# Optimization experiments

Hardware: AMD Instinct MI355X
Metric: run time of the kernel (lower is better)

## Reference

```python
import jax, jax.numpy as jnp
import numpy as np

EMB = 512
HEADS = 8


def setup_inputs() -> dict:
    key = jax.random.key(0)
    ks = jax.random.split(key, 9)
    b, t, k, h = 4, 2048, EMB, HEADS
    s = 1.0 / np.sqrt(k)
    x = jax.random.normal(ks[0], (b, t, k), dtype=jnp.float32)
    Wq = jax.random.normal(ks[1], (k, h * k), dtype=jnp.float32) * s
    bq = jnp.zeros((h * k,), dtype=jnp.float32)
    Wk = jax.random.normal(ks[2], (k, h * k), dtype=jnp.float32) * s
    bk = jnp.zeros((h * k,), dtype=jnp.float32)
    Wv = jax.random.normal(ks[3], (k, h * k), dtype=jnp.float32) * s
    bv = jnp.zeros((h * k,), dtype=jnp.float32)
    Wo = jax.random.normal(ks[4], (h * k, k), dtype=jnp.float32) * (1.0 / np.sqrt(h * k))
    bo = jnp.zeros((k,), dtype=jnp.float32)
    return {"x": x, "Wq": Wq, "bq": bq, "Wk": Wk, "bk": bk,
            "Wv": Wv, "bv": bv, "Wo": Wo, "bo": bo}


def reference(x, Wq, bq, Wk, bk, Wv, bv, Wo, bo):
    b, t, k = x.shape
    h = Wq.shape[1] // k
    scale = k ** (-0.25)  # applied to both q and k, matching /= k**(1/4)
    # projections: [b,t,k] -> [b,t,h,k] -> [b,h,t,k]
    q = (x @ Wq + bq).reshape(b, t, h, k).transpose(0, 2, 1, 3) * scale
    kk = (x @ Wk + bk).reshape(b, t, h, k).transpose(0, 2, 1, 3) * scale
    v = (x @ Wv + bv).reshape(b, t, h, k).transpose(0, 2, 1, 3)
    # attention scores [b,h,t,t]
    scores = jnp.einsum('bhqk,bhsk->bhqs', q, kk)
    w = jax.nn.softmax(scores, axis=-1)
    out = jnp.einsum('bhqs,bhsk->bhqk', w, v)  # [b,h,t,k]
    out = out.transpose(0, 2, 1, 3).reshape(b, t, h * k)
    return out @ Wo + bo
```

## Files before the change

### kernel.cpp

```cpp
#include <hip/hip_runtime.h>
#include <hip/hip_bf16.h>
#include <stdint.h>

typedef __hip_bfloat16 bf16;
typedef __bf16 bf16x8 __attribute__((ext_vector_type(8)));
typedef float floatx4 __attribute__((ext_vector_type(4)));

#define AS_LDS __attribute__((address_space(3)))
#define AS_GLB __attribute__((address_space(1)))

__device__ __forceinline__ void gload_lds16(const bf16* g, bf16* l) {
    __builtin_amdgcn_global_load_lds((const AS_GLB void*)g, (AS_LDS void*)l, 16, 0, 0);
}

__global__ void probe_dtype(const float* __restrict__ x, int* __restrict__ flag) {
    __shared__ int cnt;
    if (threadIdx.x == 0) cnt = 0;
    __syncthreads();
    int ok = 0;
    for (int i = threadIdx.x; i < 4096; i += 256) {
        float v = x[i];
        if (v == v && fabsf(v) < 1.0e3f) ok++;
    }
    atomicAdd(&cnt, ok);
    __syncthreads();
    if (threadIdx.x == 0) *flag = (cnt > 2048) ? 1 : 0;
}

__global__ __launch_bounds__(256) void convert_to_bf16(
    const void* __restrict__ in, bf16* __restrict__ out, long n,
    const int* __restrict__ flag)
{
    long i = ((long)blockIdx.x * 256 + threadIdx.x) * 8;
    if (i >= n) return;
    bf16 o[8];
    if (*flag) {
        const float* p = (const float*)in + i;
        float4 a = *(const float4*)p;
        float4 b = *(const float4*)(p + 4);
        o[0] = __float2bfloat16(a.x); o[1] = __float2bfloat16(a.y);
        o[2] = __float2bfloat16(a.z); o[3] = __float2bfloat16(a.w);
        o[4] = __float2bfloat16(b.x); o[5] = __float2bfloat16(b.y);
        o[6] = __float2bfloat16(b.z); o[7] = __float2bfloat16(b.w);
    } else {
        *(float4*)o = *(const float4*)((const bf16*)in + i);
    }
    *(float4*)&out[i] = *(float4*)o;
}

__global__ __launch_bounds__(256) void emit_out(
    const bf16* __restrict__ in, void* __restrict__ out, long n,
    const int* __restrict__ flag)
{
    long i = ((long)blockIdx.x * 256 + threadIdx.x) * 8;
    if (i >= n) return;
    bf16 v[8];
    *(float4*)v = *(const float4*)&in[i];
    if (*flag) {
        float* o = (float*)out + i;
        float4 a, b;
        a.x = __bfloat162float(v[0]); a.y = __bfloat162float(v[1]);
        a.z = __bfloat162float(v[2]); a.w = __bfloat162float(v[3]);
        b.x = __bfloat162float(v[4]); b.y = __bfloat162float(v[5]);
        b.z = __bfloat162float(v[6]); b.w = __bfloat162float(v[7]);
        *(float4*)o = a;
        *(float4*)(o + 4) = b;
    } else {
        *(float4*)((bf16*)out + i) = *(float4*)v;
    }
}

__global__ __launch_bounds__(256) void transpose_any(
    const void* __restrict__ inv, bf16* __restrict__ out,
    int ldin, int ldout, const int* __restrict__ flag)
{
    __shared__ bf16 tile[64][80];
    const int fp32 = *flag;
    const int c0 = blockIdx.x * 64;
    const int r0 = blockIdx.y * 64;
    const int tid = threadIdx.x;
#pragma unroll
    for (int it = 0; it < 2; ++it) {
        int ch = tid + it * 256;
        int r = ch >> 3, c = (ch & 7) * 8;
        long eidx = (long)(r0 + r) * ldin + (c0 + c);
        if (fp32) {
            const float* p = (const float*)inv + eidx;
            float4 a = *(const float4*)p;
            float4 b = *(const float4*)(p + 4);
            bf16 o[8];
            o[0] = __float2bfloat16(a.x); o[1] = __float2bfloat16(a.y);
            o[2] = __float2bfloat16(a.z); o[3] = __float2bfloat16(a.w);
            o[4] = __float2bfloat16(b.x); o[5] = __float2bfloat16(b.y);
            o[6] = __float2bfloat16(b.z); o[7] = __float2bfloat16(b.w);
            *(float4*)&tile[r][c] = *(float4*)o;
        } else {
            *(float4*)&tile[r][c] = *(const float4*)((const bf16*)inv + eidx);
        }
    }
    __syncthreads();
#pragma unroll
    for (int it = 0; it < 2; ++it) {
        int ch = tid + it * 256;
        int oc = ch >> 3, rb = (ch & 7) * 8;
        bf16 tmp[8];
#pragma unroll
        for (int i = 0; i < 8; ++i) tmp[i] = tile[rb + i][oc];
        *(float4*)&out[(long)(c0 + oc) * ldout + r0 + rb] = *(float4*)tmp;
    }
}

__global__ __launch_bounds__(256) void transpose_bf16(
    const bf16* __restrict__ in, bf16* __restrict__ out,
    int ldin, int ldout,
    int nz1, long in_z1, long out_z1, long in_z2, long out_z2)
{
    __shared__ bf16 tile[64][80];
    const int z = blockIdx.z;
    const int z1 = z % nz1, z2 = z / nz1;
    in  += (long)z1 * in_z1 + (long)z2 * in_z2;
    out += (long)z1 * out_z1 + (long)z2 * out_z2;
    const int c0 = blockIdx.x * 64;
    const int r0 = blockIdx.y * 64;
    const int tid = threadIdx.x;
#pragma unroll
    for (int it = 0; it < 2; ++it) {
        int ch = tid + it * 256;
        int r = ch >> 3, c = (ch & 7) * 8;
        *(float4*)&tile[r][c] = *(const float4*)&in[(long)(r0 + r) * ldin + c0 + c];
    }
    __syncthreads();
#pragma unroll
    for (int it = 0; it < 2; ++it) {
        int ch = tid + it * 256;
        int oc = ch >> 3, rb = (ch & 7) * 8;
        bf16 tmp[8];
#pragma unroll
        for (int i = 0; i < 8; ++i) tmp[i] = tile[rb + i][oc];
        *(float4*)&out[(long)(c0 + oc) * ldout + r0 + rb] = *(float4*)tmp;
    }
}

template <int MODE, bool SWAP = false>
__global__ __launch_bounds__(256) void gemm_bt(
    const bf16* __restrict__ A, const bf16* __restrict__ Bt,
    bf16* __restrict__ C, const bf16* __restrict__ bias,
    int lda, int ldb, int ldc,
    long az, long bz, long cz, int K, float scale, int qcols,
    bf16* __restrict__ Vt, int vcol0)
{
    __shared__ bf16 As[128 * 64];
    __shared__ bf16 Bs[128 * 64];

    const int tid  = threadIdx.x;
    const int lane = tid & 63;
    const int wave = tid >> 6;
    const int wx = wave & 1;
    const int wy = wave >> 1;
    const long zz = blockIdx.z;
    A  += zz * az;
    Bt += zz * bz;
    C  += zz * cz;
    const int bm = SWAP ? blockIdx.x : blockIdx.y;
    const int bn = SWAP ? blockIdx.y : blockIdx.x;
    const int m0 = bm * 128;
    const int n0 = bn * 128;

    const int lm = lane & 15;
    const int kq = (lane >> 4) * 8;

    floatx4 acc[4][4];
#pragma unroll
    for (int i = 0; i < 4; ++i)
#pragma unroll
        for (int j = 0; j < 4; ++j)
            acc[i][j] = (floatx4){0.f, 0.f, 0.f, 0.f};

    floatx4 accOnes[4];
    bf16x8 ones;
    if constexpr (MODE == 3) {
#pragma unroll
        for (int i = 0; i < 4; ++i) accOnes[i] = (floatx4){0.f, 0.f, 0.f, 0.f};
#pragma unroll
        for (int k = 0; k < 8; ++k) ones[k] = (__bf16)1.0f;
    }

    for (int kt = 0; kt < K; kt += 64) {
        __syncthreads();
#pragma unroll
        for (int it = 0; it < 4; ++it) {
            int ch = tid + it * 256;
            int r = ch >> 3;
            int c = (ch & 7) * 8;
            gload_lds16(A  + (long)(m0 + r) * lda + (kt + c), &As[ch * 8]);
            gload_lds16(Bt + (long)(n0 + r) * ldb + (kt + c), &Bs[ch * 8]);
        }
        __syncthreads();
#pragma unroll
        for (int kk = 0; kk < 64; kk += 32) {
            bf16x8 af[4], bfv[4];
#pragma unroll
            for (int i = 0; i < 4; ++i)
                af[i] = *(const bf16x8*)&As[(wy * 64 + i * 16 + lm) * 64 + kk + kq];
#pragma unroll
            for (int j = 0; j < 4; ++j)
                bfv[j] = *(const bf16x8*)&Bs[(wx * 64 + j * 16 + lm) * 64 + kk + kq];
#pragma unroll
            for (int i = 0; i < 4; ++i) {
#pragma unroll
                for (int j = 0; j < 4; ++j)
                    acc[i][j] = __builtin_amdgcn_mfma_f32_16x16x32_bf16(
                        af[i], bfv[j], acc[i][j], 0, 0, 0);
                if constexpr (MODE == 3)
                    accOnes[i] = __builtin_amdgcn_mfma_f32_16x16x32_bf16(
                        af[i], ones, accOnes[i], 0, 0, 0);
            }
        }
    }

    const int cr = (lane >> 4) * 4;
    if constexpr (MODE == 1) {
#pragma unroll
        for (int j = 0; j < 4; ++j) {
            int col = n0 + wx * 64 + j * 16 + lm;
#pragma unroll
            for (int i = 0; i < 4; ++i)
#pragma unroll
                for (int r = 0; r < 4; ++r) {
                    int row = m0 + wy * 64 + i * 16 + cr + r;
                    C[(long)row * ldc + col] = __float2bfloat16(__expf(acc[i][j][r]));
                }
        }
    } else if constexpr (MODE == 3) {
        floatx4 inv[4];
#pragma unroll
        for (int i = 0; i < 4; ++i)
#pragma unroll
            for (int r = 0; r < 4; ++r)
                inv[i][r] = 1.0f / accOnes[i][r];
#pragma unroll
        for (int j = 0; j < 4; ++j) {
            int col = n0 + wx * 64 + j * 16 + lm;
#pragma unroll
            for (int i = 0; i < 4; ++i)
#pragma unroll
                for (int r = 0; r < 4; ++r) {
                    int row = m0 + wy * 64 + i * 16 + cr + r;
                    C[(long)row * ldc + col] =
                        __float2bfloat16(acc[i][j][r] * inv[i][r]);
                }
        }
    } else if constexpr (MODE == 4) {
        if (n0 >= vcol0) {
#pragma unroll
            for (int j = 0; j < 4; ++j) {
                int col = n0 + wx * 64 + j * 16 + lm;
                float bv = __bfloat162float(bias[col]);
                int eg = col - vcol0;
                bf16* vt = Vt + ((long)(eg >> 9) * 512 + (eg & 511)) * 2048;
#pragma unroll
                for (int i = 0; i < 4; ++i) {
                    int t0 = m0 + wy * 64 + i * 16 + cr;
                    bf16 pk[4];
#pragma unroll
                    for (int r = 0; r < 4; ++r)
                        pk[r] = __float2bfloat16(acc[i][j][r] + bv);
                    *(ushort4*)&vt[t0] = *(ushort4*)pk;
                }
            }
        } else {
#pragma unroll
            for (int j = 0; j < 4; ++j) {
                int col = n0 + wx * 64 + j * 16 + lm;
                float bv = __bfloat162float(bias[col]);
                float sc = (col < qcols) ? scale : 1.0f;
#pragma unroll
                for (int i = 0; i < 4; ++i)
#pragma unroll
                    for (int r = 0; r < 4; ++r) {
                        int row = m0 + wy * 64 + i * 16 + cr + r;
                        C[(long)row * ldc + col] =
                            __float2bfloat16((acc[i][j][r] + bv) * sc);
                    }
            }
        }
    } else {
#pragma unroll
        for (int j = 0; j < 4; ++j) {
            int col = n0 + wx * 64 + j * 16 + lm;
            float bv = (MODE == 0 && bias) ? __bfloat162float(bias[col]) : 0.f;
            float sc = (col < qcols) ? scale : 1.0f;
#pragma unroll
            for (int i = 0; i < 4; ++i) {
#pragma unroll
                for (int r = 0; r < 4; ++r) {
                    int row = m0 + wy * 64 + i * 16 + cr + r;
                    long idx = (long)row * ldc + col;
                    float v;
                    if (MODE == 2) v = acc[i][j][r] + __bfloat162float(C[idx]);
                    else           v = (acc[i][j][r] + bv) * sc;
                    C[idx] = __float2bfloat16(v);
                }
            }
        }
    }
}

template <bool SWAP = false>
__global__ __launch_bounds__(256) void gemm_bt_splitk(
    const bf16* __restrict__ A, const bf16* __restrict__ Bt,
    bf16* __restrict__ P, int lda, int ldb, int ldp,
    long az, long bz, long pz, long skStride, int nsk, int Kc)
{
    __shared__ bf16 As[128 * 64];
    __shared__ bf16 Bs[128 * 64];

    const int tid  = threadIdx.x;
    const int lane = tid & 63;
    const int wave = tid >> 6;
    const int wx = wave & 1;
    const int wy = wave >> 1;
    const int zz = blockIdx.z;
    const int ks = zz % nsk;
    const int zh = zz / nsk;
    A  += (long)zh * az;
    Bt += (long)zh * bz;
    bf16* Pz = P + (long)zh * pz + (long)ks * skStride;
    const int bm = SWAP ? blockIdx.x : blockIdx.y;
    const int bn = SWAP ? blockIdx.y : blockIdx.x;
    const int m0 = bm * 128;
    const int n0 = bn * 128;
    const int k0 = ks * Kc;

    const int lm = lane & 15;
    const int kq = (lane >> 4) * 8;

    floatx4 acc[4][4];
#pragma unroll
    for (int i = 0; i < 4; ++i)
#pragma unroll
        for (int j = 0; j < 4; ++j)
            acc[i][j] = (floatx4){0.f, 0.f, 0.f, 0.f};

    for (int kt = k0; kt < k0 + Kc; kt += 64) {
        __syncthreads();
#pragma unroll
        for (int it = 0; it < 4; ++it) {
            int ch = tid + it * 256;
            int r = ch >> 3;
            int c = (ch & 7) * 8;
            gload_lds16(A  + (long)(m0 + r) * lda + (kt + c), &As[ch * 8]);
            gload_lds16(Bt + (long)(n0 + r) * ldb + (kt + c), &Bs[ch * 8]);
        }
        __syncthreads();
#pragma unroll
        for (int kk = 0; kk < 64; kk += 32) {
            bf16x8 af[4], bfv[4];
#pragma unroll
            for (int i = 0; i < 4; ++i)
                af[i] = *(const bf16x8*)&As[(wy * 64 + i * 16 + lm) * 64 + kk + kq];
#pragma unroll
            for (int j = 0; j < 4; ++j)
                bfv[j] = *(const bf16x8*)&Bs[(wx * 64 + j * 16 + lm) * 64 + kk + kq];
#pragma unroll
            for (int i = 0; i < 4; ++i)
#pragma unroll
                for (int j = 0; j < 4; ++j)
                    acc[i][j] = __builtin_amdgcn_mfma_f32_16x16x32_bf16(
                        af[i], bfv[j], acc[i][j], 0, 0, 0);
        }
    }

    const int cr = (lane >> 4) * 4;
#pragma unroll
    for (int j = 0; j < 4; ++j) {
        int col = n0 + wx * 64 + j * 16 + lm;
#pragma unroll
        for (int i = 0; i < 4; ++i)
#pragma unroll
            for (int r = 0; r < 4; ++r) {
                int row = m0 + wy * 64 + i * 16 + cr + r;
                Pz[(long)row * ldp + col] = __float2bfloat16(acc[i][j][r]);
            }
    }
}

__global__ __launch_bounds__(256) void reduce_emit(
    const bf16* __restrict__ P, const bf16* __restrict__ bias,
    void* __restrict__ out, long MN, int N,
    const int* __restrict__ flag)
{
    long i = ((long)blockIdx.x * 256 + threadIdx.x) * 8;
    if (i >= MN) return;
    bf16 bb[8], a[8], b[8];
    *(float4*)bb = *(const float4*)&bias[i & (N - 1)];
    *(float4*)a  = *(const float4*)&P[i];
    *(float4*)b  = *(const float4*)&P[MN + i];
    float s[8];
#pragma unroll
    for (int k = 0; k < 8; ++k)
        s[k] = __bfloat162float(bb[k]) + __bfloat162float(a[k]) + __bfloat162float(b[k]);
    if (*flag) {
        float* o = (float*)out + i;
        float4 lo = {s[0], s[1], s[2], s[3]};
        float4 hi = {s[4], s[5], s[6], s[7]};
        *(float4*)o = lo;
        *(float4*)(o + 4) = hi;
    } else {
        bf16 o[8];
#pragma unroll
        for (int k = 0; k < 8; ++k) o[k] = __float2bfloat16(s[k]);
        *(float4*)&((bf16*)out)[i] = *(float4*)o;
    }
}

__global__ __launch_bounds__(256) void reduce_splitk(
    const bf16* __restrict__ P, const bf16* __restrict__ bias,
    bf16* __restrict__ Out, long MN, int N, int SK)
{
    long i = ((long)blockIdx.x * 256 + threadIdx.x) * 8;
    if (i >= MN) return;
    float s[8];
    if (bias) {
        bf16 bb[8];
        *(float4*)bb = *(const float4*)&bias[i & (N - 1)];
#pragma unroll
        for (int k = 0; k < 8; ++k) s[k] = __bfloat162float(bb[k]);
    } else {
#pragma unroll
        for (int k = 0; k < 8; ++k) s[k] = 0.f;
    }
    for (int z = 0; z < SK; ++z) {
        bf16 a[8];
        *(float4*)a = *(const float4*)&P[(long)z * MN + i];
#pragma unroll
        for (int k = 0; k < 8; ++k) s[k] += __bfloat162float(a[k]);
    }
    bf16 o[8];
#pragma unroll
    for (int k = 0; k < 8; ++k) o[k] = __float2bfloat16(s[k]);
    *(float4*)&Out[i] = *(float4*)o;
}

__global__ __launch_bounds__(256) void softmax_rows2048(bf16* __restrict__ S)
{
    __shared__ float red[8];
    const long row = blockIdx.x;
    bf16* p = S + row * 2048;
    const int tid = threadIdx.x;
    float4 raw = *(const float4*)&p[tid * 8];
    bf16 vb[8];
    *(float4*)vb = raw;
    float v[8];
#pragma unroll
    for (int i = 0; i < 8; ++i) v[i] = __bfloat162float(vb[i]);
    float m = v[0];
#pragma unroll
    for (int i = 1; i < 8; ++i) m = fmaxf(m, v[i]);
#pragma unroll
    for (int o = 32; o > 0; o >>= 1) m = fmaxf(m, __shfl_xor(m, o));
    if ((tid & 63) == 0) red[tid >> 6] = m;
    __syncthreads();
    m = fmaxf(fmaxf(red[0], red[1]), fmaxf(red[2], red[3]));
    float s = 0.f;
#pragma unroll
    for (int i = 0; i < 8; ++i) { v[i] = __expf(v[i] - m); s += v[i]; }
#pragma unroll
    for (int o = 32; o > 0; o >>= 1) s += __shfl_xor(s, o);
    if ((tid & 63) == 0) red[4 + (tid >> 6)] = s;
    __syncthreads();
    s = (red[4] + red[5]) + (red[6] + red[7]);
    float inv = 1.f / s;
#pragma unroll
    for (int i = 0; i < 8; ++i) vb[i] = __float2bfloat16(v[i] * inv);
    *(float4*)&p[tid * 8] = *(float4*)vb;
}

extern "C" void kernel_launch(void* const* d_in, const int* in_sizes, int n_in,
                              void* d_out, int out_size, void* d_ws, size_t ws_size,
                              hipStream_t stream)
{
    const int Bb = 4, T = 2048, E = 512, H = 8;
    const int HE = H * E;
    const int N3 = 3 * HE;
    const int N2 = 2 * HE;
    const int M  = Bb * T;
    const long NX = (long)M * E;

    const void* xr = nullptr;
    const void* Wr[4] = {nullptr, nullptr, nullptr, nullptr};
    const void* br[3] = {nullptr, nullptr, nullptr};
    const void* bor = nullptr;
    int nw = 0, nb = 0;
    for (int i = 0; i < n_in; ++i) {
        int s = in_sizes[i];
        if      (s == (int)NX)      xr = d_in[i];
        else if (s == E * HE)       { if (nw < 4) Wr[nw++] = d_in[i]; }
        else if (s == HE)           { if (nb < 3) br[nb++] = d_in[i]; }
        else if (s == E)            bor = d_in[i];
    }
    if (!xr || nw < 4 || nb < 3 || !bor) {
        xr = d_in[0]; Wr[0] = d_in[1]; br[0] = d_in[2]; Wr[1] = d_in[3];
        br[1] = d_in[4]; Wr[2] = d_in[5]; br[2] = d_in[6]; Wr[3] = d_in[7];
        bor = d_in[8];
    }

    const float qscale = 0.04419417382415922f;
    const int   QC = 1 << 30;
    dim3 blk(256);

    bf16* pool = (bf16*)d_ws;
    int*  flag = (int*)(void*)pool;
    bf16* xc   = pool + 8;
    bf16* bqc  = xc  + NX;
    bf16* bkc  = bqc + HE;
    bf16* bvc  = bkc + HE;
    bf16* boc  = bvc + HE;
    bf16* WqT  = boc + E;
    const size_t w2m = (size_t)E * HE;
    bf16* WkT  = WqT + w2m;
    bf16* WvT  = WkT + w2m;
    bf16* WoT  = WvT + w2m;
    bf16* Ofin = WoT + w2m;
    bf16* p0   = Ofin + NX;

    const size_t wsE    = ws_size / sizeof(bf16);
    const size_t fixedE = (size_t)(p0 - pool);
    const size_t wQK   = (size_t)T * N2;
    const size_t wQKV  = (size_t)T * N3;
    const size_t wBat  = (size_t)T * HE;
    const size_t wHd   = (size_t)T * E;
    const size_t sAll  = (size_t)H * T * T;
    const size_t sOne  = (size_t)T * T;
    const size_t wBig  = (size_t)M * HE;
    const size_t needB2 = fixedE + wQK + wBat + sAll + wBig;
    const size_t needB  = fixedE + wQKV + 2 * wBat + sAll;
    const size_t needC  = fixedE + 5 * wBat + sOne;
    const size_t needD  = fixedE + 5 * wHd  + sOne;
    if (wsE < needD) return;

    probe_dtype<<<dim3(1), blk, 0, stream>>>((const float*)xr, flag);
    convert_to_bf16<<<dim3((unsigned)((NX / 8 + 255) / 256)), blk, 0, stream>>>(
        xr, xc, NX, flag);
    convert_to_bf16<<<dim3(2), blk, 0, stream>>>(br[0], bqc, HE, flag);
    convert_to_bf16<<<dim3(2), blk, 0, stream>>>(br[1], bkc, HE, flag);
    convert_to_bf16<<<dim3(2), blk, 0, stream>>>(br[2], bvc, HE, flag);
    convert_to_bf16<<<dim3(1), blk, 0, stream>>>(bor, boc, E, flag);
    transpose_any<<<dim3(HE / 64, E / 64, 1), blk, 0, stream>>>(Wr[0], WqT, HE, E, flag);
    transpose_any<<<dim3(HE / 64, E / 64, 1), blk, 0, stream>>>(Wr[1], WkT, HE, E, flag);
    transpose_any<<<dim3(HE / 64, E / 64, 1), blk, 0, stream>>>(Wr[2], WvT, HE, E, flag);
    transpose_any<<<dim3(E / 64, HE / 64, 1), blk, 0, stream>>>(Wr[3], WoT, E, HE, flag);

    if (wsE >= needB2) {
        bf16* QKb = p0;
        bf16* Vtb = QKb + wQK;
        bf16* S   = Vtb + wBat;
        bf16* Oatt = S + sAll;

        for (int b = 0; b < Bb; ++b) {
            const bf16* xb = xc + (size_t)b * T * E;
            gemm_bt<4><<<dim3(N3 / 128, T / 128, 1), blk, 0, stream>>>(
                xb, WqT, QKb, bqc, E, E, N2, 0, 0, 0, E, qscale, HE, Vtb, N2);
            gemm_bt<1><<<dim3(T / 128, T / 128, H), blk, 0, stream>>>(
                QKb, QKb + HE, S, nullptr, N2, N2, T,
                (long)E, (long)E, (long)T * T, E, 1.f, QC, nullptr, 0);
            gemm_bt<3, true><<<dim3(T / 128, E / 128, H), blk, 0, stream>>>(
                S, Vtb, Oatt + (size_t)b * T * HE, nullptr, T, T, HE,
                (long)T * T, (long)E * T, (long)E, T, 1.f, QC, nullptr, 0);
        }
        gemm_bt_splitk<true><<<dim3(M / 128, E / 128, 2), blk, 0, stream>>>(
            Oatt, WoT, QKb, HE, HE, E, 0, 0, 0, (long)M * E, 2, HE / 2);
        reduce_emit<<<dim3((unsigned)((NX / 8 + 255) / 256)), blk, 0, stream>>>(
            QKb, boc, d_out, NX, E, flag);
        return;
    }

    if (wsE >= needB) {
        bf16* QKVb = p0;
        bf16* Vtb  = QKVb + wQKV;
        bf16* Oatt = Vtb + wBat;
        bf16* S    = Oatt + wBat;

        for (int b = 0; b < Bb; ++b) {
            const bf16* xb = xc + (size_t)b * T * E;
            gemm_bt<0><<<dim3(N3 / 128, T / 128, 1), blk, 0, stream>>>(
                xb, WqT, QKVb, bqc, E, E, N3, 0, 0, 0, E, qscale, HE, nullptr, 0);
            transpose_bf16<<<dim3(E / 64, T / 64, H), blk, 0, stream>>>(
                QKVb + 2 * HE, Vtb, N3, T, H, (long)E, (long)E * T, 0, 0);
            gemm_bt<0><<<dim3(T / 128, T / 128, H), blk, 0, stream>>>(
                QKVb, QKVb + HE, S, nullptr, N3, N3, T,
                (long)E, (long)E, (long)T * T, E, 1.f, QC, nullptr, 0);
            softmax_rows2048<<<dim3(H * T, 1, 1), blk, 0, stream>>>(S);
            gemm_bt<0><<<dim3(E / 128, T / 128, H), blk, 0, stream>>>(
                S, Vtb, Oatt, nullptr, T, T, HE,
                (long)T * T, (long)E * T, (long)E, T, 1.f, QC, nullptr, 0);
            gemm_bt_splitk<false><<<dim3(E / 128, T / 128, 8), blk, 0, stream>>>(
                Oatt, WoT, (bf16*)S, HE, HE, E, 0, 0, 0, (long)T * E, 8, HE / 8);
            reduce_splitk<<<dim3((unsigned)(((long)T * E / 8 + 255) / 256)), blk, 0, stream>>>(
                (bf16*)S, boc, Ofin + (size_t)b * T * E, (long)T * E, E, 8);
        }
    } else if (wsE >= needC) {
        bf16* Qb  = p0;
        bf16* Kb  = Qb  + wBat;
        bf16* Vb  = Kb  + wBat;
        bf16* Vtb = Vb  + wBat;
        bf16* Ob  = Vtb + wBat;
        bf16* S   = Ob  + wBat;

        for (int b = 0; b < Bb; ++b) {
            const bf16* xb = xc + (size_t)b * T * E;
            gemm_bt<0><<<dim3(HE / 128, T / 128, 1), blk, 0, stream>>>(
                xb, WqT, Qb, bqc, E, E, HE, 0, 0, 0, E, qscale, QC, nullptr, 0);
            gemm_bt<0><<<dim3(HE / 128, T / 128, 1), blk, 0, stream>>>(
                xb, WkT, Kb, bkc, E, E, HE, 0, 0, 0, E, 1.f, QC, nullptr, 0);
            gemm_bt<0><<<dim3(HE / 128, T / 128, 1), blk, 0, stream>>>(
                xb, WvT, Vb, bvc, E, E, HE, 0, 0, 0, E, 1.f, QC, nullptr, 0);
            transpose_bf16<<<dim3(E / 64, T / 64, H), blk, 0, stream>>>(
                Vb, Vtb, HE, T, H, (long)E, (long)E * T, 0, 0);
            for (int h = 0; h < H; ++h) {
                gemm_bt<0><<<dim3(T / 128, T / 128, 1), blk, 0, stream>>>(
                    Qb + (size_t)h * E, Kb + (size_t)h * E, S, nullptr,
                    HE, HE, T, 0, 0, 0, E, 1.f, QC, nullptr, 0);
                softmax_rows2048<<<dim3(T, 1, 1), blk, 0, stream>>>(S);
                gemm_bt<0><<<dim3(E / 128, T / 128, 1), blk, 0, stream>>>(
                    S, Vtb + (size_t)h * E * T, Ob + (size_t)h * E, nullptr,
                    T, T, HE, 0, 0, 0, T, 1.f, QC, nullptr, 0);
            }
            gemm_bt<0><<<dim3(E / 128, T / 128, 1), blk, 0, stream>>>(
                Ob, WoT, Ofin + (size_t)b * T * E, boc,
                HE, HE, E, 0, 0, 0, HE, 1.f, QC, nullptr, 0);
        }
    } else {
        bf16* Qh  = p0;
        bf16* Kh  = Qh  + wHd;
        bf16* Vh  = Kh  + wHd;
        bf16* Vth = Vh  + wHd;
        bf16* Oh  = Vth + wHd;
        bf16* S   = Oh  + wHd;

        for (int b = 0; b < Bb; ++b) {
            const bf16* xb = xc + (size_t)b * T * E;
            bf16* outb = Ofin + (size_t)b * T * E;
            for (int h = 0; h < H; ++h) {
                const size_t hw = (size_t)h * E * E;
                gemm_bt<0><<<dim3(E / 128, T / 128, 1), blk, 0, stream>>>(
                    xb, WqT + hw, Qh, bqc + (size_t)h * E, E, E, E,
                    0, 0, 0, E, qscale, QC, nullptr, 0);
                gemm_bt<0><<<dim3(E / 128, T / 128, 1), blk, 0, stream>>>(
                    xb, WkT + hw, Kh, bkc + (size_t)h * E, E, E, E,
                    0, 0, 0, E, 1.f, QC, nullptr, 0);
                gemm_bt<0><<<dim3(E / 128, T / 128, 1), blk, 0, stream>>>(
                    xb, WvT + hw, Vh, bvc + (size_t)h * E, E, E, E,
                    0, 0, 0, E, 1.f, QC, nullptr, 0);
                transpose_bf16<<<dim3(E / 64, T / 64, 1), blk, 0, stream>>>(
                    Vh, Vth, E, T, 1, 0, 0, 0, 0);
                gemm_bt<0><<<dim3(T / 128, T / 128, 1), blk, 0, stream>>>(
                    Qh, Kh, S, nullptr, E, E, T, 0, 0, 0, E, 1.f, QC, nullptr, 0);
                softmax_rows2048<<<dim3(T, 1, 1), blk, 0, stream>>>(S);
                gemm_bt<0><<<dim3(E / 128, T / 128, 1), blk, 0, stream>>>(
                    S, Vth, Oh, nullptr, T, T, E, 0, 0, 0, T, 1.f, QC, nullptr, 0);
                if (h == 0)
                    gemm_bt<0><<<dim3(E / 128, T / 128, 1), blk, 0, stream>>>(
                        Oh, WoT, outb, boc, E, HE, E, 0, 0, 0, E, 1.f, QC, nullptr, 0);
                else
                    gemm_bt<2><<<dim3(E / 128, T / 128, 1), blk, 0, stream>>>(
                        Oh, WoT + (size_t)h * E, outb, nullptr,
                        E, HE, E, 0, 0, 0, E, 1.f, QC, nullptr, 0);
            }
        }
    }

    emit_out<<<dim3((unsigned)((NX / 8 + 255) / 256)), blk, 0, stream>>>(
        Ofin, d_out, NX, flag);
}
```

Before: 914.7 us.

## Add 256x256-tile 8-wave GEMM with staged LDS pipeline for QKV and scores

Adds a new gemm256 kernel that uses 256x256 output tiles, 512 threads (8 waves) and double-buffered LDS split into K-halves. Global-to-LDS direct loads are interleaved with MFMA phases under explicit barriers, waitcnts and setprio. It replaces the 128x128 gemm_bt for the QKV projection and the QK^T score GEMMs. The goal is more data reuse per tile and better overlap of loads with MFMA. The cost is higher register and LDS pressure, a grid with fewer blocks, and fragile manual scheduling.

Result: slower. 975.2 us (+6.6%).

```diff
diff --git a/kernel.cpp b/kernel.cpp
--- a/kernel.cpp
+++ b/kernel.cpp
@@ -141,6 +141,181 @@
     }
 }
 
+template <int MODE>
+__global__ __launch_bounds__(512, 2) void gemm256(
+    const bf16* __restrict__ A, const bf16* __restrict__ Bt,
+    bf16* __restrict__ C, const bf16* __restrict__ bias,
+    int lda, int ldb, int ldc,
+    long az, long bz, long cz, int K, float scale, int qcols,
+    bf16* __restrict__ Vt, int vcol0)
+{
+    __shared__ bf16 AsL[2][2][256 * 32];
+    __shared__ bf16 BsL[2][2][256 * 32];
+
+    const int tid  = threadIdx.x;
+    const int lane = tid & 63;
+    const int wave = tid >> 6;
+    const int wr = wave >> 2;
+    const int wc = wave & 3;
+    const int lm = lane & 15;
+    const int cl = lane >> 4;
+    const long zz = blockIdx.z;
+    A  += zz * az;
+    Bt += zz * bz;
+    C  += zz * cz;
+    const int m0 = blockIdx.y * 256;
+    const int n0 = blockIdx.x * 256;
+
+    int offA[8], offB[4];
+#pragma unroll
+    for (int i = 0; i < 8; ++i) {
+        int row = wr * 128 + i * 16 + lm;
+        offA[i] = row * 32 + ((cl ^ ((row >> 1) & 3)) << 3);
+    }
+#pragma unroll
+    for (int j = 0; j < 4; ++j) {
+        int row = wc * 64 + j * 16 + lm;
+        offB[j] = row * 32 + ((cl ^ ((row >> 1) & 3)) << 3);
+    }
+
+    const int sr = lane >> 2;
+    const int sc = lane & 3;
+    const int NT = K >> 6;
+
+    floatx4 acc[8][4];
+#pragma unroll
+    for (int i = 0; i < 8; ++i)
+#pragma unroll
+        for (int j = 0; j < 4; ++j)
+            acc[i][j] = (floatx4){0.f, 0.f, 0.f, 0.f};
+
+    auto stageU = [&](int which, int t, int kh) {
+        if (t >= NT) return;
+        const bf16* G = which ? Bt : A;
+        const int ldg  = which ? ldb : lda;
+        const int g0   = which ? n0 : m0;
+        bf16* lb = which ? &BsL[t & 1][kh][0] : &AsL[t & 1][kh][0];
+        const int kcol = t * 64 + kh * 32;
+#pragma unroll
+        for (int ii = 0; ii < 2; ++ii) {
+            int row = ii * 128 + wave * 16 + sr;
+            int cg  = sc ^ ((row >> 1) & 3);
+            gload_lds16(G + (long)(g0 + row) * ldg + kcol + cg * 8,
+                        lb + row * 32 + sc * 8);
+        }
+    };
+
+    bf16x8 af[8], bfv[2];
+    auto dsA = [&](int b, int kh) {
+        const bf16* p = &AsL[b][kh][0];
+#pragma unroll
+        for (int i = 0; i < 8; ++i) af[i] = *(const bf16x8*)(p + offA[i]);
+    };
+    auto dsB = [&](int b, int kh, int nh) {
+        const bf16* p = &BsL[b][kh][0];
+        bfv[0] = *(const bf16x8*)(p + offB[nh * 2]);
+        bfv[1] = *(const bf16x8*)(p + offB[nh * 2 + 1]);
+    };
+    auto mfmaQ = [&](int nh) {
+        __builtin_amdgcn_s_setprio(1);
+#pragma unroll
+        for (int i = 0; i < 8; ++i) {
+            acc[i][nh * 2] = __builtin_amdgcn_mfma_f32_16x16x32_bf16(
+                af[i], bfv[0], acc[i][nh * 2], 0, 0, 0);
+            acc[i][nh * 2 + 1] = __builtin_amdgcn_mfma_f32_16x16x32_bf16(
+                af[i], bfv[1], acc[i][nh * 2 + 1], 0, 0, 0);
+        }
+        __builtin_amdgcn_s_setprio(0);
+    };
+
+#define BAR    __builtin_amdgcn_s_barrier()
+#define SBZ    __builtin_amdgcn_sched_barrier(0)
+#define LGKM0  do { asm volatile("s_waitcnt lgkmcnt(0)" ::: "memory"); SBZ; } while (0)
+#define VM(n)  do { asm volatile("s_waitcnt vmcnt(" #n ")" ::: "memory"); SBZ; } while (0)
+
+    stageU(0, 0, 0); stageU(1, 0, 0); stageU(0, 0, 1); stageU(1, 0, 1);
+    stageU(0, 1, 0); stageU(1, 1, 0);
+    VM(4);
+    BAR;
+
+    for (int t0 = 0; t0 < NT; t0 += 2) {
+        const bool last = (t0 + 2 >= NT);
+        dsA(0, 0); dsB(0, 0, 0); stageU(0, t0 + 1, 1);
+        BAR; LGKM0; mfmaQ(0); BAR;
+        dsB(0, 0, 1); stageU(1, t0 + 1, 1);
+        BAR; LGKM0; mfmaQ(1); BAR;
+        dsA(0, 1); dsB(0, 1, 0); stageU(0, t0 + 2, 0);
+        BAR; LGKM0; mfmaQ(0); BAR;
+        dsB(0, 1, 1); stageU(1, t0 + 2, 0);
+        BAR; LGKM0; mfmaQ(1);
+        if (last) { VM(0); } else { VM(4); }
+        BAR;
+        dsA(1, 0); dsB(1, 0, 0); stageU(0, t0 + 2, 1);
+        BAR; LGKM0; mfmaQ(0); BAR;
+        dsB(1, 0, 1); stageU(1, t0 + 2, 1);
+        BAR; LGKM0; mfmaQ(1); BAR;
+        dsA(1, 1); dsB(1, 1, 0); stageU(0, t0 + 3, 0);
+        BAR; LGKM0; mfmaQ(0); BAR;
+        dsB(1, 1, 1); stageU(1, t0 + 3, 0);
+        BAR; LGKM0; mfmaQ(1);
+        if (!last) { VM(4); }
+        BAR;
+    }
+#undef BAR
+#undef SBZ
+#undef LGKM0
+#undef VM
+
+    const int cr = (lane >> 4) * 4;
+    if constexpr (MODE == 1) {
+#pragma unroll
+        for (int j = 0; j < 4; ++j) {
+            int col = n0 + wc * 64 + j * 16 + lm;
+#pragma unroll
+            for (int i = 0; i < 8; ++i)
+#pragma unroll
+                for (int r = 0; r < 4; ++r) {
+                    int row = m0 + wr * 128 + i * 16 + cr + r;
+                    C[(long)row * ldc + col] = __float2bfloat16(__expf(acc[i][j][r]));
+                }
+        }
+    } else {
+        if (n0 >= vcol0) {
+#pragma unroll
+            for (int j = 0; j < 4; ++j) {
+                int col = n0 + wc * 64 + j * 16 + lm;
+                float bv = __bfloat162float(bias[col]);
+                int eg = col - vcol0;
+                bf16* vt = Vt + ((long)(eg >> 9) * 512 + (eg & 511)) * 2048;
+#pragma unroll
+                for (int i = 0; i < 8; ++i) {
+                    int t0v = m0 + wr * 128 + i * 16 + cr;
+                    bf16 pk[4];
+#pragma unroll
+                    for (int r = 0; r < 4; ++r)
+                        pk[r] = __float2bfloat16(acc[i][j][r] + bv);
+                    *(ushort4*)&vt[t0v] = *(ushort4*)pk;
+                }
+            }
+        } else {
+#pragma unroll
+            for (int j = 0; j < 4; ++j) {
+                int col = n0 + wc * 64 + j * 16 + lm;
+                float bv = __bfloat162float(bias[col]);
+                float sc2 = (col < qcols) ? scale : 1.0f;
+#pragma unroll
+                for (int i = 0; i < 8; ++i)
+#pragma unroll
+                    for (int r = 0; r < 4; ++r) {
+                        int row = m0 + wr * 128 + i * 16 + cr + r;
+                        C[(long)row * ldc + col] =
+                            __float2bfloat16((acc[i][j][r] + bv) * sc2);
+                    }
+            }
+        }
+    }
+}
+
 template <int MODE, bool SWAP = false>
 __global__ __launch_bounds__(256) void gemm_bt(
     const bf16* __restrict__ A, const bf16* __restrict__ Bt,
@@ -559,9 +734,9 @@
 
         for (int b = 0; b < Bb; ++b) {
             const bf16* xb = xc + (size_t)b * T * E;
-            gemm_bt<4><<<dim3(N3 / 128, T / 128, 1), blk, 0, stream>>>(
+            gemm256<4><<<dim3(N3 / 256, T / 256, 1), dim3(512), 0, stream>>>(
                 xb, WqT, QKb, bqc, E, E, N2, 0, 0, 0, E, qscale, HE, Vtb, N2);
-            gemm_bt<1><<<dim3(T / 128, T / 128, H), blk, 0, stream>>>(
+            gemm256<1><<<dim3(T / 256, T / 256, H), dim3(512), 0, stream>>>(
                 QKb, QKb + HE, S, nullptr, N2, N2, T,
                 (long)E, (long)E, (long)T * T, E, 1.f, QC, nullptr, 0);
             gemm_bt<3, true><<<dim3(T / 128, E / 128, H), blk, 0, stream>>>(
```
